# Kernel optimization log

Hardware: AMD Instinct MI355X
Metric: run time of the kernel (lower is better)

## Reference

```python
import jax, jax.numpy as jnp
import numpy as np

N_NODES = 100000
N_EDGES = 600000
IN_CH = 128
HID = 64
NEG_SLOPE = 0.01  # nn.LeakyReLU default


def setup_inputs() -> dict:
    key = jax.random.key(0)
    k1, k2, k3, k4, k5, k6, k7, k8 = jax.random.split(key, 8)
    s1 = 1.0 / np.sqrt(IN_CH)
    s2 = 1.0 / np.sqrt(HID)
    return {
        "z": jax.random.normal(k1, (N_NODES, IN_CH), dtype=jnp.float32),
        "edge_index": jax.random.randint(k2, (2, N_EDGES), 0, N_NODES, dtype=jnp.int64),
        "W1l": jax.random.uniform(k3, (HID, IN_CH), jnp.float32, -s1, s1),
        "b1l": jax.random.uniform(k4, (HID,), jnp.float32, -s1, s1),
        "W1r": jax.random.uniform(k5, (HID, IN_CH), jnp.float32, -s1, s1),
        "b1r": jax.random.uniform(k6, (HID,), jnp.float32, -s1, s1),
        "W2": jax.random.uniform(k7, (1, HID), jnp.float32, -s2, s2),
        "b2": jax.random.uniform(k8, (1,), jnp.float32, -s2, s2),
    }


def reference(z, edge_index, W1l, b1l, W1r, b1r, W2, b2):
    # gather src/dst node features: [E, in_ch]
    zl = z[edge_index[0]]
    zr = z[edge_index[1]]
    # dual linear + add: [E, hid]
    h = jnp.einsum('ei,hi->eh', zl, W1l) + b1l + jnp.einsum('ei,hi->eh', zr, W1r) + b1r
    h = jnp.where(h >= 0, h, NEG_SLOPE * h)  # LeakyReLU
    out = jnp.einsum('eh,oh->eo', h, W2) + b2  # [E, 1]
    return jax.nn.sigmoid(out)
```

## Files before the change

### kernel.cpp

```cpp
#include <hip/hip_runtime.h>
#include <math.h>

#define N_NODES 100000
#define N_EDGES 600000
#define IN_CH 128
#define HID 64
#define NEG_SLOPE 0.01f

typedef float4 f4;
typedef unsigned short u16;
typedef unsigned int u32;
typedef __attribute__((ext_vector_type(8))) short bf16x8;
typedef __attribute__((ext_vector_type(4))) float f32x4;

__device__ __forceinline__ float lrelu(float x) {
    return fmaxf(x, NEG_SLOPE * x);
}
__device__ __forceinline__ float uasf(u32 w) { return __uint_as_float(w); }
__device__ __forceinline__ u16 f2bf(float f) {
    u32 x = __float_as_uint(f);
    return (u16)((x + 0x7fffu + ((x >> 16) & 1u)) >> 16);
}
__device__ __forceinline__ u32 pack2(float a, float b) {
    return (u32)f2bf(a) | ((u32)f2bf(b) << 16);
}

__device__ __forceinline__ int load_idx(const void* ei, int is64, int pos) {
    if (is64) return (int)((const long long*)ei)[pos];
    return ((const int*)ei)[pos];
}

__global__ __launch_bounds__(256) void node_proj_kernel(
    const float* __restrict__ z, const float* __restrict__ W1l,
    const float* __restrict__ b1l, const float* __restrict__ W1r,
    const float* __restrict__ b1r, const u32* __restrict__ ei_words,
    int* __restrict__ flag, u16* __restrict__ pcomb) {
    __shared__ uint4 wt[128 * 16];
    __shared__ uint4 zt[64 * 16];
    __shared__ u32 red;

    const int tid = threadIdx.x;

    if (blockIdx.x == 0) {
        if (tid == 0) red = 0u;
        __syncthreads();
        u32 acc = 0u;
        #pragma unroll
        for (int i = 0; i < 8; ++i)
            acc |= ei_words[(i * 256 + tid) * 2 + 1];
        atomicOr(&red, acc);
        __syncthreads();
        if (tid == 0) *flag = (red == 0u) ? 1 : 0;
    }

    #pragma unroll
    for (int i = 0; i < 8; ++i) {
        int gidx = tid + i * 256;
        int row = gidx >> 4, gr = gidx & 15;
        const float* wsrc = (row < 64) ? (W1l + row * IN_CH)
                                       : (W1r + (row - 64) * IN_CH);
        f4 a = ((const f4*)wsrc)[gr * 2];
        f4 b = ((const f4*)wsrc)[gr * 2 + 1];
        uint4 p;
        p.x = pack2(a.x, a.y); p.y = pack2(a.z, a.w);
        p.z = pack2(b.x, b.y); p.w = pack2(b.z, b.w);
        wt[(row << 4) | (gr ^ (row & 15))] = p;
    }

    const int base = blockIdx.x * 64;
    #pragma unroll
    for (int i = 0; i < 4; ++i) {
        int gidx = tid + i * 256;
        int row = gidx >> 4, gr = gidx & 15;
        int node = base + row;
        if (node >= N_NODES) node = N_NODES - 1;
        f4 a = ((const f4*)z)[node * 32 + gr * 2];
        f4 b = ((const f4*)z)[node * 32 + gr * 2 + 1];
        uint4 p;
        p.x = pack2(a.x, a.y); p.y = pack2(a.z, a.w);
        p.z = pack2(b.x, b.y); p.w = pack2(b.z, b.w);
        zt[(row << 4) | (gr ^ (row & 15))] = p;
    }
    __syncthreads();

    const int wave = tid >> 6, lane = tid & 63;
    const int m = lane & 15, g = lane >> 4;

    f32x4 acc[8];
    #pragma unroll
    for (int c = 0; c < 8; ++c) acc[c] = {0.f, 0.f, 0.f, 0.f};

    const int zrow = (wave << 4) | m;
    #pragma unroll
    for (int kk = 0; kk < 4; ++kk) {
        int gran = (kk << 2) | g;
        bf16x8 zf = *(const bf16x8*)&zt[(zrow << 4) | (gran ^ m)];
        #pragma unroll
        for (int c = 0; c < 8; ++c) {
            int wrow = (c << 4) | m;
            bf16x8 wf = *(const bf16x8*)&wt[(wrow << 4) | (gran ^ m)];
            acc[c] = __builtin_amdgcn_mfma_f32_16x16x32_bf16(wf, zf, acc[c],
                                                             0, 0, 0);
        }
    }

    const int node = base + (wave << 4) + m;
    if (node < N_NODES) {
        u16* orow = pcomb + (size_t)node * 128;
        #pragma unroll
        for (int c = 0; c < 8; ++c) {
            int col = (c << 4) + (g << 2);
            const float* bsrc = (col < 64) ? (b1l + col) : (b1r + (col - 64));
            f4 bb = *(const f4*)bsrc;
            uint2 v;
            v.x = pack2(acc[c][0] + bb.x, acc[c][1] + bb.y);
            v.y = pack2(acc[c][2] + bb.z, acc[c][3] + bb.w);
            *(uint2*)(orow + col) = v;
        }
    }
}

__global__ __launch_bounds__(256) void edge_kernel(
    const void* __restrict__ ei, const int* __restrict__ flag,
    const u16* __restrict__ pcomb, const float* __restrict__ W2,
    const float* __restrict__ b2, float* __restrict__ out) {
    int t = blockIdx.x * 256 + threadIdx.x;
    int e = t >> 3;
    int c = t & 7;
    if (e >= N_EDGES) return;
    const int is64 = *flag;
    int src = load_idx(ei, is64, e);
    int dst = load_idx(ei, is64, N_EDGES + e);
    uint4 a = ((const uint4*)pcomb)[src * 16 + c];
    uint4 b = ((const uint4*)pcomb)[dst * 16 + 8 + c];
    f4 w0 = ((const f4*)W2)[c * 2];
    f4 w1 = ((const f4*)W2)[c * 2 + 1];
    float s;
    s  = lrelu(uasf(a.x << 16) + uasf(b.x << 16)) * w0.x;
    s += lrelu(uasf(a.x & 0xffff0000u) + uasf(b.x & 0xffff0000u)) * w0.y;
    s += lrelu(uasf(a.y << 16) + uasf(b.y << 16)) * w0.z;
    s += lrelu(uasf(a.y & 0xffff0000u) + uasf(b.y & 0xffff0000u)) * w0.w;
    s += lrelu(uasf(a.z << 16) + uasf(b.z << 16)) * w1.x;
    s += lrelu(uasf(a.z & 0xffff0000u) + uasf(b.z & 0xffff0000u)) * w1.y;
    s += lrelu(uasf(a.w << 16) + uasf(b.w << 16)) * w1.z;
    s += lrelu(uasf(a.w & 0xffff0000u) + uasf(b.w & 0xffff0000u)) * w1.w;
    s += __shfl_xor(s, 4, 8);
    s += __shfl_xor(s, 2, 8);
    s += __shfl_xor(s, 1, 8);
    if (c == 0) {
        float x = s + b2[0];
        out[e] = 1.f / (1.f + __expf(-x));
    }
}

__global__ void detect_idx_kernel(const u32* __restrict__ ei_words,
                                  int* __restrict__ flag) {
    __shared__ u32 red;
    if (threadIdx.x == 0) red = 0u;
    __syncthreads();
    u32 acc = 0u;
    #pragma unroll
    for (int i = 0; i < 8; ++i)
        acc |= ei_words[(i * 256 + threadIdx.x) * 2 + 1];
    atomicOr(&red, acc);
    __syncthreads();
    if (threadIdx.x == 0) *flag = (red == 0u) ? 1 : 0;
}

__global__ __launch_bounds__(256) void edge_fallback_kernel(
    const float* __restrict__ z, const void* __restrict__ ei,
    const int* __restrict__ flag, const float* __restrict__ W1l,
    const float* __restrict__ b1l, const float* __restrict__ W1r,
    const float* __restrict__ b1r, const float* __restrict__ W2,
    const float* __restrict__ b2, float* __restrict__ out) {
    __shared__ f4 Wl4[64 * 32];
    __shared__ f4 Wr4[64 * 32];
    const int tid = threadIdx.x;
    #pragma unroll
    for (int i = 0; i < 8; ++i) {
        int gg = tid + i * 256;
        int h = gg >> 5, v = gg & 31;
        int slot = (h << 5) | (v ^ (h & 7));
        Wl4[slot] = ((const f4*)W1l)[gg];
        Wr4[slot] = ((const f4*)W1r)[gg];
    }
    __syncthreads();
    const int wave = tid >> 6, lane = tid & 63;
    int e = blockIdx.x * 4 + wave;
    if (e >= N_EDGES) return;
    const int is64 = (flag != nullptr) ? *flag : 0;
    int src = load_idx(ei, is64, e);
    int dst = load_idx(ei, is64, N_EDGES + e);
    float accl = 0.f, accr = 0.f;
    #pragma unroll 4
    for (int v = 0; v < 32; ++v) {
        f4 wl = Wl4[(lane << 5) | (v ^ (lane & 7))];
        f4 wr = Wr4[(lane << 5) | (v ^ (lane & 7))];
        f4 zl = ((const f4*)z)[src * 32 + v];
        f4 zr = ((const f4*)z)[dst * 32 + v];
        accl += wl.x * zl.x + wl.y * zl.y + wl.z * zl.z + wl.w * zl.w;
        accr += wr.x * zr.x + wr.y * zr.y + wr.z * zr.z + wr.w * zr.w;
    }
    float h = lrelu(accl + b1l[lane] + accr + b1r[lane]) * W2[lane];
    #pragma unroll
    for (int off = 32; off; off >>= 1) h += __shfl_xor(h, off, 64);
    if (lane == 0) out[e] = 1.f / (1.f + __expf(-(h + b2[0])));
}

extern "C" void kernel_launch(void* const* d_in, const int* in_sizes, int n_in,
                              void* d_out, int out_size, void* d_ws,
                              size_t ws_size, hipStream_t stream) {
    const float* z   = (const float*)d_in[0];
    const void*  ei  = d_in[1];
    const float* W1l = (const float*)d_in[2];
    const float* b1l = (const float*)d_in[3];
    const float* W1r = (const float*)d_in[4];
    const float* b1r = (const float*)d_in[5];
    const float* W2  = (const float*)d_in[6];
    const float* b2  = (const float*)d_in[7];
    float* out = (float*)d_out;

    const size_t pcomb_bytes = (size_t)N_NODES * 128 * sizeof(u16);
    const size_t need = pcomb_bytes + 256;

    if (ws_size >= need) {
        u16* pcomb = (u16*)d_ws;
        int* flag = (int*)((char*)d_ws + pcomb_bytes);
        node_proj_kernel<<<(N_NODES + 63) / 64, 256, 0, stream>>>(
            z, W1l, b1l, W1r, b1r, (const u32*)ei, flag, pcomb);
        edge_kernel<<<(N_EDGES * 8 + 255) / 256, 256, 0, stream>>>(
            ei, flag, pcomb, W2, b2, out);
    } else if (ws_size >= 256) {
        int* flag = (int*)d_ws;
        detect_idx_kernel<<<1, 256, 0, stream>>>((const u32*)ei, flag);
        edge_fallback_kernel<<<(N_EDGES + 3) / 4, 256, 0, stream>>>(
            z, ei, flag, W1l, b1l, W1r, b1r, W2, b2, out);
    } else {
        edge_fallback_kernel<<<(N_EDGES + 3) / 4, 256, 0, stream>>>(
            z, ei, nullptr, W1l, b1l, W1r, b1r, W2, b2, out);
    }
}
```

Baseline: 47.13 us.

## Repartition node projection MFMA tiling, use packed bf16 convert, two edges per thread

The node projection now splits output columns across waves instead of node rows, so each wave loads 4 z fragments and 2 weight fragments per k-step rather than 8 weight fragments. The software round-to-nearest bf16 packing is replaced with the hardware v_cvt_pk_bf16_f32 instruction. The edge kernel handles two edges per 8-lane group, with vectorized index loads and a float2 output store. This raises memory-level parallelism and halves the thread count, at the cost of more registers per thread and an inline-asm dependency on a specific ISA.

```diff
diff --git a/kernel.cpp b/kernel.cpp
--- a/kernel.cpp
+++ b/kernel.cpp
@@ -17,12 +17,15 @@
     return fmaxf(x, NEG_SLOPE * x);
 }
 __device__ __forceinline__ float uasf(u32 w) { return __uint_as_float(w); }
+
+__device__ __forceinline__ u32 cvt_pk(float lo, float hi) {
+    u32 r;
+    asm("v_cvt_pk_bf16_f32 %0, %1, %2" : "=v"(r) : "v"(lo), "v"(hi));
+    return r;
+}
 __device__ __forceinline__ u16 f2bf(float f) {
     u32 x = __float_as_uint(f);
     return (u16)((x + 0x7fffu + ((x >> 16) & 1u)) >> 16);
-}
-__device__ __forceinline__ u32 pack2(float a, float b) {
-    return (u32)f2bf(a) | ((u32)f2bf(b) << 16);
 }
 
 __device__ __forceinline__ int load_idx(const void* ei, int is64, int pos) {
@@ -62,8 +65,8 @@
         f4 a = ((const f4*)wsrc)[gr * 2];
         f4 b = ((const f4*)wsrc)[gr * 2 + 1];
         uint4 p;
-        p.x = pack2(a.x, a.y); p.y = pack2(a.z, a.w);
-        p.z = pack2(b.x, b.y); p.w = pack2(b.z, b.w);
+        p.x = cvt_pk(a.x, a.y); p.y = cvt_pk(a.z, a.w);
+        p.z = cvt_pk(b.x, b.y); p.w = cvt_pk(b.z, b.w);
         wt[(row << 4) | (gr ^ (row & 15))] = p;
     }
 
@@ -77,8 +80,8 @@
         f4 a = ((const f4*)z)[node * 32 + gr * 2];
         f4 b = ((const f4*)z)[node * 32 + gr * 2 + 1];
         uint4 p;
-        p.x = pack2(a.x, a.y); p.y = pack2(a.z, a.w);
-        p.z = pack2(b.x, b.y); p.w = pack2(b.z, b.w);
+        p.x = cvt_pk(a.x, a.y); p.y = cvt_pk(a.z, a.w);
+        p.z = cvt_pk(b.x, b.y); p.w = cvt_pk(b.z, b.w);
         zt[(row << 4) | (gr ^ (row & 15))] = p;
     }
     __syncthreads();
@@ -86,55 +89,52 @@
     const int wave = tid >> 6, lane = tid & 63;
     const int m = lane & 15, g = lane >> 4;
 
-    f32x4 acc[8];
-    #pragma unroll
-    for (int c = 0; c < 8; ++c) acc[c] = {0.f, 0.f, 0.f, 0.f};
-
-    const int zrow = (wave << 4) | m;
+    f32x4 acc[4][2];
+    #pragma unroll
+    for (int n4 = 0; n4 < 4; ++n4)
+        #pragma unroll
+        for (int c2 = 0; c2 < 2; ++c2) acc[n4][c2] = {0.f, 0.f, 0.f, 0.f};
+
     #pragma unroll
     for (int kk = 0; kk < 4; ++kk) {
-        int gran = (kk << 2) | g;
-        bf16x8 zf = *(const bf16x8*)&zt[(zrow << 4) | (gran ^ m)];
-        #pragma unroll
-        for (int c = 0; c < 8; ++c) {
-            int wrow = (c << 4) | m;
-            bf16x8 wf = *(const bf16x8*)&wt[(wrow << 4) | (gran ^ m)];
-            acc[c] = __builtin_amdgcn_mfma_f32_16x16x32_bf16(wf, zf, acc[c],
-                                                             0, 0, 0);
+        const int gran = (kk << 2) | g;
+        bf16x8 zf[4], wf[2];
+        #pragma unroll
+        for (int n4 = 0; n4 < 4; ++n4)
+            zf[n4] = *(const bf16x8*)&zt[((((n4 << 4) | m)) << 4) | (gran ^ m)];
+        #pragma unroll
+        for (int c2 = 0; c2 < 2; ++c2) {
+            int R = (wave << 5) + (c2 << 4) + m;
+            wf[c2] = *(const bf16x8*)&wt[(R << 4) | (gran ^ m)];
         }
-    }
-
-    const int node = base + (wave << 4) + m;
-    if (node < N_NODES) {
-        u16* orow = pcomb + (size_t)node * 128;
-        #pragma unroll
-        for (int c = 0; c < 8; ++c) {
-            int col = (c << 4) + (g << 2);
-            const float* bsrc = (col < 64) ? (b1l + col) : (b1r + (col - 64));
-            f4 bb = *(const f4*)bsrc;
-            uint2 v;
-            v.x = pack2(acc[c][0] + bb.x, acc[c][1] + bb.y);
-            v.y = pack2(acc[c][2] + bb.z, acc[c][3] + bb.w);
-            *(uint2*)(orow + col) = v;
+        #pragma unroll
+        for (int n4 = 0; n4 < 4; ++n4)
+            #pragma unroll
+            for (int c2 = 0; c2 < 2; ++c2)
+                acc[n4][c2] = __builtin_amdgcn_mfma_f32_16x16x32_bf16(
+                    wf[c2], zf[n4], acc[n4][c2], 0, 0, 0);
+    }
+
+    const int colbase = wave << 5;
+    #pragma unroll
+    for (int c2 = 0; c2 < 2; ++c2) {
+        const int col0 = colbase + (c2 << 4) + (g << 2);
+        const float* bsrc = (colbase < 64) ? (b1l + col0) : (b1r + col0 - 64);
+        f4 bb = *(const f4*)bsrc;
+        #pragma unroll
+        for (int n4 = 0; n4 < 4; ++n4) {
+            int node = base + (n4 << 4) + m;
+            if (node < N_NODES) {
+                uint2 v;
+                v.x = cvt_pk(acc[n4][c2][0] + bb.x, acc[n4][c2][1] + bb.y);
+                v.y = cvt_pk(acc[n4][c2][2] + bb.z, acc[n4][c2][3] + bb.w);
+                *(uint2*)(pcomb + (size_t)node * 128 + col0) = v;
+            }
         }
     }
 }
 
-__global__ __launch_bounds__(256) void edge_kernel(
-    const void* __restrict__ ei, const int* __restrict__ flag,
-    const u16* __restrict__ pcomb, const float* __restrict__ W2,
-    const float* __restrict__ b2, float* __restrict__ out) {
-    int t = blockIdx.x * 256 + threadIdx.x;
-    int e = t >> 3;
-    int c = t & 7;
-    if (e >= N_EDGES) return;
-    const int is64 = *flag;
-    int src = load_idx(ei, is64, e);
-    int dst = load_idx(ei, is64, N_EDGES + e);
-    uint4 a = ((const uint4*)pcomb)[src * 16 + c];
-    uint4 b = ((const uint4*)pcomb)[dst * 16 + 8 + c];
-    f4 w0 = ((const f4*)W2)[c * 2];
-    f4 w1 = ((const f4*)W2)[c * 2 + 1];
+__device__ __forceinline__ float edot(uint4 a, uint4 b, f4 w0, f4 w1) {
     float s;
     s  = lrelu(uasf(a.x << 16) + uasf(b.x << 16)) * w0.x;
     s += lrelu(uasf(a.x & 0xffff0000u) + uasf(b.x & 0xffff0000u)) * w0.y;
@@ -144,12 +144,51 @@
     s += lrelu(uasf(a.z & 0xffff0000u) + uasf(b.z & 0xffff0000u)) * w1.y;
     s += lrelu(uasf(a.w << 16) + uasf(b.w << 16)) * w1.z;
     s += lrelu(uasf(a.w & 0xffff0000u) + uasf(b.w & 0xffff0000u)) * w1.w;
-    s += __shfl_xor(s, 4, 8);
-    s += __shfl_xor(s, 2, 8);
-    s += __shfl_xor(s, 1, 8);
+    return s;
+}
+
+__global__ __launch_bounds__(256) void edge_kernel(
+    const void* __restrict__ ei, const int* __restrict__ flag,
+    const u16* __restrict__ pcomb, const float* __restrict__ W2,
+    const float* __restrict__ b2, float* __restrict__ out) {
+    int t = blockIdx.x * 256 + threadIdx.x;
+    int pair = t >> 3;
+    int c = t & 7;
+    if (pair >= N_EDGES / 2) return;
+    const int is64 = *flag;
+    int s0, s1, d0, d1;
+    if (is64) {
+        const longlong2* p = (const longlong2*)ei;
+        longlong2 sp = p[pair];
+        longlong2 dp = p[N_EDGES / 2 + pair];
+        s0 = (int)sp.x; s1 = (int)sp.y; d0 = (int)dp.x; d1 = (int)dp.y;
+    } else {
+        const int2* p = (const int2*)ei;
+        int2 sp = p[pair];
+        int2 dp = p[N_EDGES / 2 + pair];
+        s0 = sp.x; s1 = sp.y; d0 = dp.x; d1 = dp.y;
+    }
+    const uint4* pc4 = (const uint4*)pcomb;
+    uint4 a0 = pc4[s0 * 16 + c];
+    uint4 b0 = pc4[d0 * 16 + 8 + c];
+    uint4 a1 = pc4[s1 * 16 + c];
+    uint4 b1 = pc4[d1 * 16 + 8 + c];
+    f4 w0 = ((const f4*)W2)[c * 2];
+    f4 w1 = ((const f4*)W2)[c * 2 + 1];
+    float r0 = edot(a0, b0, w0, w1);
+    float r1 = edot(a1, b1, w0, w1);
+    r0 += __shfl_xor(r0, 4, 8);
+    r0 += __shfl_xor(r0, 2, 8);
+    r0 += __shfl_xor(r0, 1, 8);
+    r1 += __shfl_xor(r1, 4, 8);
+    r1 += __shfl_xor(r1, 2, 8);
+    r1 += __shfl_xor(r1, 1, 8);
     if (c == 0) {
-        float x = s + b2[0];
-        out[e] = 1.f / (1.f + __expf(-x));
+        float bb = b2[0];
+        float2 o;
+        o.x = 1.f / (1.f + __expf(-(r0 + bb)));
+        o.y = 1.f / (1.f + __expf(-(r1 + bb)));
+        *(float2*)(out + pair * 2) = o;
     }
 }
 
@@ -228,7 +267,7 @@
         int* flag = (int*)((char*)d_ws + pcomb_bytes);
         node_proj_kernel<<<(N_NODES + 63) / 64, 256, 0, stream>>>(
             z, W1l, b1l, W1r, b1r, (const u32*)ei, flag, pcomb);
-        edge_kernel<<<(N_EDGES * 8 + 255) / 256, 256, 0, stream>>>(
+        edge_kernel<<<(N_EDGES / 2 * 8 + 255) / 256, 256, 0, stream>>>(
             ei, flag, pcomb, W2, b2, out);
     } else if (ws_size >= 256) {
         int* flag = (int*)d_ws;
```

Measured after the change: 45.67 us. 1.03x faster.
